# Kernel tuning notes

Measured on AMD Instinct MI355X. Metric: run time of the kernel, lower is better.

Reference implementation:

```python
import jax, jax.numpy as jnp
import numpy as np

DIM_V = 512
H = 8
EPS = 1e-5

def _layernorm(x, g, b):
    mu = jnp.mean(x, axis=-1, keepdims=True)
    var = jnp.var(x, axis=-1, keepdims=True)
    return (x - mu) * jax.lax.rsqrt(var + EPS) * g + b

def setup_inputs() -> dict:
    key = jax.random.key(0)
    ks = jax.random.split(key, 10)
    B, Nq, Nk, dq, dk, dv = 8, 1024, 1024, 512, 512, DIM_V
    def lin(k, fan_in, shape):
        bound = 1.0 / np.sqrt(fan_in)
        return jax.random.uniform(k, shape, jnp.float32, -bound, bound)
    return {
        "Q": jax.random.normal(ks[0], (B, Nq, dq), jnp.float32),
        "K": jax.random.normal(ks[1], (B, Nk, dk), jnp.float32),
        "Wq": lin(ks[2], dq, (dv, dq)), "bq": lin(ks[3], dq, (dv,)),
        "Wk": lin(ks[4], dk, (dv, dk)), "bk": lin(ks[5], dk, (dv,)),
        "Wv": lin(ks[6], dk, (dv, dk)), "bv": lin(ks[7], dk, (dv,)),
        "Wo": lin(ks[8], dv, (dv, dv)), "bo": lin(ks[9], dv, (dv,)),
        "g0": jnp.ones((dv,), jnp.float32), "beta0": jnp.zeros((dv,), jnp.float32),
        "g1": jnp.ones((dv,), jnp.float32), "beta1": jnp.zeros((dv,), jnp.float32),
    }

def reference(Q, K, Wq, bq, Wk, bk, Wv, bv, Wo, bo, g0, beta0, g1, beta1):
    B, Nq, _ = Q.shape
    Nk = K.shape[1]
    d_h = DIM_V // H
    Qp = Q @ Wq.T + bq            # [B,Nq,dv]
    Kp = K @ Wk.T + bk            # [B,Nk,dv]
    Vp = K @ Wv.T + bv            # [B,Nk,dv]
    # split heads along feature dim (matches torch split(dim_split,2)+cat(0))
    Qh = Qp.reshape(B, Nq, H, d_h).transpose(0, 2, 1, 3)  # [B,H,Nq,dh]
    Kh = Kp.reshape(B, Nk, H, d_h).transpose(0, 2, 1, 3)
    Vh = Vp.reshape(B, Nk, H, d_h).transpose(0, 2, 1, 3)
    # NOTE: original scales by sqrt(dim_V), the FULL model dim
    scores = jnp.einsum('bhnd,bhmd->bhnm', Qh, Kh) / jnp.sqrt(jnp.float32(DIM_V))
    A = jax.nn.softmax(scores, axis=-1)                   # [B,H,Nq,Nk]
    Oh = Qh + jnp.einsum('bhnm,bhmd->bhnd', A, Vh)        # residual on projected Q
    O = Oh.transpose(0, 2, 1, 3).reshape(B, Nq, DIM_V)
    O = _layernorm(O, g0, beta0)
    O = O + jax.nn.relu(O @ Wo.T + bo)
    O = _layernorm(O, g1, beta1)
    return O
```

## Files before the change

kernel.cpp:

```cpp
#include <hip/hip_runtime.h>
#include <hip/hip_bf16.h>

typedef __hip_bfloat16 bf16;
typedef short bf16x8 __attribute__((ext_vector_type(8)));
typedef float f32x4 __attribute__((ext_vector_type(4)));
typedef unsigned int u32;

static __device__ __forceinline__ float bfu2f(unsigned short u) { return __uint_as_float((u32)u << 16); }
static __device__ __forceinline__ u32 pack2(float a, float b) {
    return (u32)__bfloat16_as_ushort(__float2bfloat16(a))
         | ((u32)__bfloat16_as_ushort(__float2bfloat16(b)) << 16);
}
static __device__ __forceinline__ float wave_sum(float v) {
    #pragma unroll
    for (int off = 32; off > 0; off >>= 1) v += __shfl_xor(v, off);
    return v;
}

static __device__ __forceinline__ void gll16(const bf16* g, bf16* l) {
    __builtin_amdgcn_global_load_lds((const __attribute__((address_space(1))) void*)g,
                                     (__attribute__((address_space(3))) void*)l,
                                     16, 0, 0);
}

__global__ __launch_bounds__(256) void castall(const float* __restrict__ Q,  const float* __restrict__ K,
                                               const float* __restrict__ Wq, const float* __restrict__ Wk,
                                               const float* __restrict__ Wv, const float* __restrict__ Wo,
                                               bf16* __restrict__ dQ,  bf16* __restrict__ dK,
                                               bf16* __restrict__ dWq, bf16* __restrict__ dWk,
                                               bf16* __restrict__ dWv, bf16* __restrict__ dWo)
{
    const int b = blockIdx.x;
    const float* src; bf16* dst; size_t off;
    if (b < 1024)      { src = Q;  dst = dQ;  off = (size_t)b * 4096; }
    else if (b < 2048) { src = K;  dst = dK;  off = (size_t)(b - 1024) * 4096; }
    else {
        const int wb = b - 2048, wi = wb >> 6;
        off = (size_t)(wb & 63) * 4096;
        src = wi == 0 ? Wq : wi == 1 ? Wk : wi == 2 ? Wv : Wo;
        dst = wi == 0 ? dWq : wi == 1 ? dWk : wi == 2 ? dWv : dWo;
    }
    const size_t p = off + threadIdx.x * 16;
    const float4 v0 = *(const float4*)(src + p);
    const float4 v1 = *(const float4*)(src + p + 4);
    const float4 v2 = *(const float4*)(src + p + 8);
    const float4 v3 = *(const float4*)(src + p + 12);
    uint4 o0, o1;
    o0.x = pack2(v0.x, v0.y); o0.y = pack2(v0.z, v0.w);
    o0.z = pack2(v1.x, v1.y); o0.w = pack2(v1.z, v1.w);
    o1.x = pack2(v2.x, v2.y); o1.y = pack2(v2.z, v2.w);
    o1.z = pack2(v3.x, v3.y); o1.w = pack2(v3.z, v3.w);
    *(uint4*)(dst + p)     = o0;
    *(uint4*)(dst + p + 8) = o1;
}

__global__ __launch_bounds__(256) void gemm_qkv(const bf16* __restrict__ Aq, const bf16* __restrict__ Ak,
                                                const bf16* __restrict__ Wq, const bf16* __restrict__ Wk,
                                                const bf16* __restrict__ Wv,
                                                const float* __restrict__ bq, const float* __restrict__ bk,
                                                const float* __restrict__ bv,
                                                bf16* __restrict__ oQ, bf16* __restrict__ oK,
                                                bf16* __restrict__ oV)
{
    __shared__ bf16 Xs[128 * 64];
    __shared__ bf16 Ws[128 * 64];

    const int tid = threadIdx.x, lane = tid & 63, wave = tid >> 6;
    const int yy = blockIdx.y, wi = yy >> 2;
    const bf16* A     = wi == 0 ? Aq : Ak;
    const bf16* W     = wi == 0 ? Wq : wi == 1 ? Wk : Wv;
    const float* bias = wi == 0 ? bq : wi == 1 ? bk : bv;
    bf16* out         = wi == 0 ? oQ : wi == 1 ? oK : oV;
    const bool vmode  = (wi == 2);
    const int bm = blockIdx.x * 128;
    const int bn = (yy & 3) * 128;

    const int srow = tid >> 3;
    const int sg8  = (((tid & 7) ^ (srow & 7)) * 8);
    const int wm = (wave >> 1) * 64, wn = (wave & 1) * 64;
    const int fr = lane & 15, fq = lane >> 4;

    f32x4 acc[4][4] = {};
    const bf16* Ap = A + (size_t)(bm + srow) * 512 + sg8;
    const bf16* Wp = W + (size_t)(bn + srow) * 512 + sg8;
    const int ld = 8 * tid;

    for (int k0 = 0; k0 < 512; k0 += 64) {
        __syncthreads();
        #pragma unroll
        for (int c = 0; c < 4; c++) {
            gll16(Ap + k0 + (size_t)(32 * c) * 512, Xs + ld + 2048 * c);
            gll16(Wp + k0 + (size_t)(32 * c) * 512, Ws + ld + 2048 * c);
        }
        __syncthreads();

        #pragma unroll
        for (int c2 = 0; c2 < 2; c2++) {
            bf16x8 fx[4], fw[4];
            #pragma unroll
            for (int i = 0; i < 4; i++) {
                const int rx = wm + 16 * i + fr;
                const int rw = wn + 16 * i + fr;
                fx[i] = *(const bf16x8*)(&Xs[rx * 64 + (((c2 * 4 + fq) ^ (rx & 7)) * 8)]);
                fw[i] = *(const bf16x8*)(&Ws[rw * 64 + (((c2 * 4 + fq) ^ (rw & 7)) * 8)]);
            }
            if (vmode) {
                #pragma unroll
                for (int i = 0; i < 4; i++)
                    #pragma unroll
                    for (int j = 0; j < 4; j++)
                        acc[i][j] = __builtin_amdgcn_mfma_f32_16x16x32_bf16(fx[i], fw[j], acc[i][j], 0, 0, 0);
            } else {
                #pragma unroll
                for (int i = 0; i < 4; i++)
                    #pragma unroll
                    for (int j = 0; j < 4; j++)
                        acc[i][j] = __builtin_amdgcn_mfma_f32_16x16x32_bf16(fw[i], fx[j], acc[i][j], 0, 0, 0);
            }
        }
    }

    if (!vmode) {
        #pragma unroll
        for (int i = 0; i < 4; i++) {
            const int colb = bn + wn + 16 * i + 4 * fq;
            const float4 b4 = *(const float4*)(bias + colb);
            const int h = colb >> 6, d0 = colb & 63;
            #pragma unroll
            for (int j = 0; j < 4; j++) {
                const int n = bm + wm + 16 * j + fr;
                const int b = n >> 10, nn = n & 1023;
                uint2 pk;
                pk.x = pack2(acc[i][j][0] + b4.x, acc[i][j][1] + b4.y);
                pk.y = pack2(acc[i][j][2] + b4.z, acc[i][j][3] + b4.w);
                *(uint2*)(out + ((size_t)(b * 8 + h) * 1024 + nn) * 64 + d0) = pk;
            }
        }
    } else {
        #pragma unroll
        for (int i = 0; i < 4; i++) {
            const int n0 = bm + wm + 16 * i + 4 * fq;
            const int b = n0 >> 10, nn = n0 & 1023;
            #pragma unroll
            for (int j = 0; j < 4; j++) {
                const int col = bn + wn + 16 * j + fr;
                const float bv2 = bias[col];
                const int h = col >> 6, d = col & 63;
                uint2 pk;
                pk.x = pack2(acc[i][j][0] + bv2, acc[i][j][1] + bv2);
                pk.y = pack2(acc[i][j][2] + bv2, acc[i][j][3] + bv2);
                *(uint2*)(out + ((size_t)(b * 8 + h) * 64 + d) * 1024 + nn) = pk;
            }
        }
    }
}

__global__ __launch_bounds__(256) void gemm_o(const bf16* __restrict__ A,
                                              const bf16* __restrict__ W,
                                              const float* __restrict__ bias,
                                              bf16* __restrict__ out)
{
    __shared__ bf16 Xs[64 * 64];
    __shared__ bf16 Ws[128 * 64];

    const int tid = threadIdx.x, lane = tid & 63, wave = tid >> 6;
    const int bm = blockIdx.x * 64;
    const int bn = blockIdx.y * 128;

    const int srow = tid >> 3;
    const int sg8  = (((tid & 7) ^ (srow & 7)) * 8);
    const int wn = wave * 32;
    const int fr = lane & 15, fq = lane >> 4;

    f32x4 acc[2][4] = {};
    const bf16* Ap = A + (size_t)(bm + srow) * 512 + sg8;
    const bf16* Wp = W + (size_t)(bn + srow) * 512 + sg8;
    const int ld = 8 * tid;

    for (int k0 = 0; k0 < 512; k0 += 64) {
        __syncthreads();
        #pragma unroll
        for (int c = 0; c < 2; c++)
            gll16(Ap + k0 + (size_t)(32 * c) * 512, Xs + ld + 2048 * c);
        #pragma unroll
        for (int c = 0; c < 4; c++)
            gll16(Wp + k0 + (size_t)(32 * c) * 512, Ws + ld + 2048 * c);
        __syncthreads();

        #pragma unroll
        for (int c2 = 0; c2 < 2; c2++) {
            bf16x8 fx[4], fw[2];
            #pragma unroll
            for (int j = 0; j < 4; j++) {
                const int rx = 16 * j + fr;
                fx[j] = *(const bf16x8*)(&Xs[rx * 64 + (((c2 * 4 + fq) ^ (rx & 7)) * 8)]);
            }
            #pragma unroll
            for (int i = 0; i < 2; i++) {
                const int rw = wn + 16 * i + fr;
                fw[i] = *(const bf16x8*)(&Ws[rw * 64 + (((c2 * 4 + fq) ^ (rw & 7)) * 8)]);
            }
            #pragma unroll
            for (int i = 0; i < 2; i++)
                #pragma unroll
                for (int j = 0; j < 4; j++)
                    acc[i][j] = __builtin_amdgcn_mfma_f32_16x16x32_bf16(fw[i], fx[j], acc[i][j], 0, 0, 0);
        }
    }

    #pragma unroll
    for (int i = 0; i < 2; i++) {
        const int colb = bn + wn + 16 * i + 4 * fq;
        const float4 b4 = *(const float4*)(bias + colb);
        #pragma unroll
        for (int j = 0; j < 4; j++) {
            const int row = bm + 16 * j + fr;
            uint2 pk;
            pk.x = pack2(acc[i][j][0] + b4.x, acc[i][j][1] + b4.y);
            pk.y = pack2(acc[i][j][2] + b4.z, acc[i][j][3] + b4.w);
            *(uint2*)(out + (size_t)row * 512 + colb) = pk;
        }
    }
}

__global__ __launch_bounds__(256) void attn_mfma(const bf16* __restrict__ Qh,
                                                 const bf16* __restrict__ Kh,
                                                 const bf16* __restrict__ VhT,
                                                 bf16* __restrict__ Oc)
{
    __shared__ bf16 Ks[64 * 64];
    __shared__ bf16 Vs[64 * 64];
    __shared__ bf16 Ps[4][16 * 72];

    const int tid = threadIdx.x, lane = tid & 63, w = tid >> 6;
    const int id = blockIdx.x;
    const int bh = (id & 7) * 8 + (id >> 7);
    const int wq = ((id >> 3) & 15) * 64 + w * 16;

    const bf16* Qb = Qh  + ((size_t)bh * 1024 + wq) * 64;
    const bf16* Kb = Kh  + (size_t)bh * 1024 * 64;
    const bf16* Vb = VhT + (size_t)bh * 64 * 1024;

    const int fl = lane & 15, fq = lane >> 4;
    const int flk = fl & 7;
    const int gA = (fq ^ flk) * 8;
    const int gB = ((4 | fq) ^ flk) * 8;

    bf16x8 qf[2];
    qf[0] = *(const bf16x8*)(Qb + fl * 64 + fq * 8);
    qf[1] = *(const bf16x8*)(Qb + fl * 64 + 32 + fq * 8);

    f32x4 o[4] = {};
    float lsum = 0.f;
    const float sc2 = 0.04419417382415922f * 1.4426950408889634f;

    const int srow = tid >> 3;
    const int sg8  = (((tid & 7) ^ (srow & 7)) * 8);
    const bf16* KbR  = Kb + (size_t)srow * 64 + sg8;
    const bf16* VbR0 = Vb + (size_t)srow * 1024 + sg8;
    const bf16* VbR1 = Vb + (size_t)(srow + 32) * 1024 + sg8;
    const int ld = 8 * tid;

    for (int kt = 0; kt < 16; kt++) {
        const int m0 = kt * 64;
        __syncthreads();
        gll16(KbR + (size_t)m0 * 64,        Ks + ld);
        gll16(KbR + (size_t)(m0 + 32) * 64, Ks + 2048 + ld);
        gll16(VbR0 + m0,                    Vs + ld);
        gll16(VbR1 + m0,                    Vs + 2048 + ld);
        __syncthreads();

        bf16x8 kf[4][2];
        #pragma unroll
        for (int tm = 0; tm < 4; tm++) {
            kf[tm][0] = *(const bf16x8*)(&Ks[(16 * tm + fl) * 64 + gA]);
            kf[tm][1] = *(const bf16x8*)(&Ks[(16 * tm + fl) * 64 + gB]);
        }

        f32x4 st[4] = {};
        #pragma unroll
        for (int tm = 0; tm < 4; tm++) {
            st[tm] = __builtin_amdgcn_mfma_f32_16x16x32_bf16(kf[tm][0], qf[0], st[tm], 0, 0, 0);
            st[tm] = __builtin_amdgcn_mfma_f32_16x16x32_bf16(kf[tm][1], qf[1], st[tm], 0, 0, 0);
        }
        #pragma unroll
        for (int tm = 0; tm < 4; tm++) {
            float p0 = __builtin_amdgcn_exp2f(st[tm][0] * sc2);
            float p1 = __builtin_amdgcn_exp2f(st[tm][1] * sc2);
            float p2 = __builtin_amdgcn_exp2f(st[tm][2] * sc2);
            float p3 = __builtin_amdgcn_exp2f(st[tm][3] * sc2);
            lsum += (p0 + p1) + (p2 + p3);
            uint2 pk;
            pk.x = pack2(p0, p1);
            pk.y = pack2(p2, p3);
            *(uint2*)(&Ps[w][fl * 72 + 16 * tm + fq * 4]) = pk;
        }

        bf16x8 vf[4][2];
        #pragma unroll
        for (int jd = 0; jd < 4; jd++) {
            vf[jd][0] = *(const bf16x8*)(&Vs[(16 * jd + fl) * 64 + gA]);
            vf[jd][1] = *(const bf16x8*)(&Vs[(16 * jd + fl) * 64 + gB]);
        }
        bf16x8 pf0 = *(const bf16x8*)(&Ps[w][fl * 72 + fq * 8]);
        bf16x8 pf1 = *(const bf16x8*)(&Ps[w][fl * 72 + 32 + fq * 8]);
        #pragma unroll
        for (int jd = 0; jd < 4; jd++) {
            o[jd] = __builtin_amdgcn_mfma_f32_16x16x32_bf16(vf[jd][0], pf0, o[jd], 0, 0, 0);
            o[jd] = __builtin_amdgcn_mfma_f32_16x16x32_bf16(vf[jd][1], pf1, o[jd], 0, 0, 0);
        }
    }

    const int b = bh >> 3, h = bh & 7;
    float ls = lsum;
    ls += __shfl_xor(ls, 16);
    ls += __shfl_xor(ls, 32);
    const float linv = 1.f / ls;
    const size_t obase = ((size_t)(b * 1024 + wq + fl)) * 512 + h * 64;
    #pragma unroll
    for (int jd = 0; jd < 4; jd++) {
        const ushort4 qr = *(const ushort4*)(Qb + fl * 64 + 16 * jd + fq * 4);
        uint2 w2;
        w2.x = pack2(o[jd][0] * linv + bfu2f(qr.x), o[jd][1] * linv + bfu2f(qr.y));
        w2.y = pack2(o[jd][2] * linv + bfu2f(qr.z), o[jd][3] * linv + bfu2f(qr.w));
        *(uint2*)(&Oc[obase + 16 * jd + fq * 4]) = w2;
    }
}

__global__ __launch_bounds__(256) void ln0(const bf16* __restrict__ X,
                                           const float* __restrict__ g,
                                           const float* __restrict__ be,
                                           bf16* __restrict__ Y)
{
    const int lane = threadIdx.x & 63;
    const int row = blockIdx.x * 4 + (threadIdx.x >> 6);
    const size_t base = (size_t)row * 512 + lane * 8;
    const bf16x8 xv = *(const bf16x8*)(X + base);
    float x[8];
    #pragma unroll
    for (int j = 0; j < 8; j++) x[j] = bfu2f((unsigned short)xv[j]);
    float s = 0.f, s2 = 0.f;
    #pragma unroll
    for (int j = 0; j < 8; j++) { s += x[j]; s2 += x[j] * x[j]; }
    s = wave_sum(s); s2 = wave_sum(s2);
    const float mean = s * (1.f / 512.f);
    const float var = s2 * (1.f / 512.f) - mean * mean;
    const float rs = rsqrtf(fmaxf(var, 0.f) + 1e-5f);
    const float4 gv0 = *(const float4*)(g + lane * 8);
    const float4 gv1 = *(const float4*)(g + lane * 8 + 4);
    const float4 bv0 = *(const float4*)(be + lane * 8);
    const float4 bv1 = *(const float4*)(be + lane * 8 + 4);
    uint4 ov;
    ov.x = pack2((x[0]-mean)*rs*gv0.x + bv0.x, (x[1]-mean)*rs*gv0.y + bv0.y);
    ov.y = pack2((x[2]-mean)*rs*gv0.z + bv0.z, (x[3]-mean)*rs*gv0.w + bv0.w);
    ov.z = pack2((x[4]-mean)*rs*gv1.x + bv1.x, (x[5]-mean)*rs*gv1.y + bv1.y);
    ov.w = pack2((x[6]-mean)*rs*gv1.z + bv1.z, (x[7]-mean)*rs*gv1.w + bv1.w);
    *(uint4*)(Y + base) = ov;
}

__global__ __launch_bounds__(256) void ln1(const bf16* __restrict__ X,
                                           const bf16* __restrict__ R,
                                           const float* __restrict__ g,
                                           const float* __restrict__ be,
                                           float* __restrict__ Y)
{
    const int lane = threadIdx.x & 63;
    const int row = blockIdx.x * 4 + (threadIdx.x >> 6);
    const size_t base = (size_t)row * 512 + lane * 8;
    const bf16x8 xv = *(const bf16x8*)(X + base);
    const bf16x8 rv = *(const bf16x8*)(R + base);
    float x[8];
    #pragma unroll
    for (int j = 0; j < 8; j++)
        x[j] = bfu2f((unsigned short)rv[j]) + fmaxf(bfu2f((unsigned short)xv[j]), 0.f);
    float s = 0.f, s2 = 0.f;
    #pragma unroll
    for (int j = 0; j < 8; j++) { s += x[j]; s2 += x[j] * x[j]; }
    s = wave_sum(s); s2 = wave_sum(s2);
    const float mean = s * (1.f / 512.f);
    const float var = s2 * (1.f / 512.f) - mean * mean;
    const float rs = rsqrtf(fmaxf(var, 0.f) + 1e-5f);
    const float4 gv0 = *(const float4*)(g + lane * 8);
    const float4 gv1 = *(const float4*)(g + lane * 8 + 4);
    const float4 bv0 = *(const float4*)(be + lane * 8);
    const float4 bv1 = *(const float4*)(be + lane * 8 + 4);
    float4 y0, y1;
    y0.x = (x[0]-mean)*rs*gv0.x + bv0.x; y0.y = (x[1]-mean)*rs*gv0.y + bv0.y;
    y0.z = (x[2]-mean)*rs*gv0.z + bv0.z; y0.w = (x[3]-mean)*rs*gv0.w + bv0.w;
    y1.x = (x[4]-mean)*rs*gv1.x + bv1.x; y1.y = (x[5]-mean)*rs*gv1.y + bv1.y;
    y1.z = (x[6]-mean)*rs*gv1.z + bv1.z; y1.w = (x[7]-mean)*rs*gv1.w + bv1.w;
    *(float4*)(Y + base)     = y0;
    *(float4*)(Y + base + 4) = y1;
}

extern "C" void kernel_launch(void* const* d_in, const int* in_sizes, int n_in,
                              void* d_out, int out_size, void* d_ws, size_t ws_size,
                              hipStream_t stream)
{
    const float* Q   = (const float*)d_in[0];
    const float* K   = (const float*)d_in[1];
    const float* Wq  = (const float*)d_in[2];
    const float* bq  = (const float*)d_in[3];
    const float* Wk  = (const float*)d_in[4];
    const float* bk  = (const float*)d_in[5];
    const float* Wv  = (const float*)d_in[6];
    const float* bv  = (const float*)d_in[7];
    const float* Wo  = (const float*)d_in[8];
    const float* bo  = (const float*)d_in[9];
    const float* g0  = (const float*)d_in[10];
    const float* be0 = (const float*)d_in[11];
    const float* g1  = (const float*)d_in[12];
    const float* be1 = (const float*)d_in[13];
    float* out = (float*)d_out;

    const size_t NQK = (size_t)8 * 1024 * 512;
    const size_t NW  = (size_t)512 * 512;
    bf16* ws   = (bf16*)d_ws;
    bf16* cQ   = ws;
    bf16* cK   = cQ + NQK;
    bf16* cWq  = cK + NQK;
    bf16* cWk  = cWq + NW;
    bf16* cWv  = cWk + NW;
    bf16* cWo  = cWv + NW;
    bf16* pQh  = cWo + NW;
    bf16* pKh  = pQh + NQK;
    bf16* pVhT = pKh + NQK;
    bf16* pOc  = (bf16*)d_out;
    bf16* pO1  = pKh;
    bf16* pTmp = pQh;

    castall<<<2304, 256, 0, stream>>>(Q, K, Wq, Wk, Wv, Wo, cQ, cK, cWq, cWk, cWv, cWo);
    gemm_qkv<<<dim3(64, 12), 256, 0, stream>>>(cQ, cK, cWq, cWk, cWv, bq, bk, bv, pQh, pKh, pVhT);
    attn_mfma<<<1024, 256, 0, stream>>>(pQh, pKh, pVhT, pOc);
    ln0<<<2048, 256, 0, stream>>>(pOc, g0, be0, pO1);
    gemm_o<<<dim3(128, 4), 256, 0, stream>>>(pO1, cWo, bo, pTmp);
    ln1<<<2048, 256, 0, stream>>>(pTmp, pO1, g1, be1, out);
}
```

Measured before the change: 187.5 us.

## Fuse output projection GEMM with relu residual and final layernorm

```diff
diff --git a/kernel.cpp b/kernel.cpp
--- a/kernel.cpp
+++ b/kernel.cpp
@@ -151,74 +151,6 @@
                 pk.y = pack2(acc[i][j][2] + bv2, acc[i][j][3] + bv2);
                 *(uint2*)(out + ((size_t)(b * 8 + h) * 64 + d) * 1024 + nn) = pk;
             }
-        }
-    }
-}
-
-__global__ __launch_bounds__(256) void gemm_o(const bf16* __restrict__ A,
-                                              const bf16* __restrict__ W,
-                                              const float* __restrict__ bias,
-                                              bf16* __restrict__ out)
-{
-    __shared__ bf16 Xs[64 * 64];
-    __shared__ bf16 Ws[128 * 64];
-
-    const int tid = threadIdx.x, lane = tid & 63, wave = tid >> 6;
-    const int bm = blockIdx.x * 64;
-    const int bn = blockIdx.y * 128;
-
-    const int srow = tid >> 3;
-    const int sg8  = (((tid & 7) ^ (srow & 7)) * 8);
-    const int wn = wave * 32;
-    const int fr = lane & 15, fq = lane >> 4;
-
-    f32x4 acc[2][4] = {};
-    const bf16* Ap = A + (size_t)(bm + srow) * 512 + sg8;
-    const bf16* Wp = W + (size_t)(bn + srow) * 512 + sg8;
-    const int ld = 8 * tid;
-
-    for (int k0 = 0; k0 < 512; k0 += 64) {
-        __syncthreads();
-        #pragma unroll
-        for (int c = 0; c < 2; c++)
-            gll16(Ap + k0 + (size_t)(32 * c) * 512, Xs + ld + 2048 * c);
-        #pragma unroll
-        for (int c = 0; c < 4; c++)
-            gll16(Wp + k0 + (size_t)(32 * c) * 512, Ws + ld + 2048 * c);
-        __syncthreads();
-
-        #pragma unroll
-        for (int c2 = 0; c2 < 2; c2++) {
-            bf16x8 fx[4], fw[2];
-            #pragma unroll
-            for (int j = 0; j < 4; j++) {
-                const int rx = 16 * j + fr;
-                fx[j] = *(const bf16x8*)(&Xs[rx * 64 + (((c2 * 4 + fq) ^ (rx & 7)) * 8)]);
-            }
-            #pragma unroll
-            for (int i = 0; i < 2; i++) {
-                const int rw = wn + 16 * i + fr;
-                fw[i] = *(const bf16x8*)(&Ws[rw * 64 + (((c2 * 4 + fq) ^ (rw & 7)) * 8)]);
-            }
-            #pragma unroll
-            for (int i = 0; i < 2; i++)
-                #pragma unroll
-                for (int j = 0; j < 4; j++)
-                    acc[i][j] = __builtin_amdgcn_mfma_f32_16x16x32_bf16(fw[i], fx[j], acc[i][j], 0, 0, 0);
-        }
-    }
-
-    #pragma unroll
-    for (int i = 0; i < 2; i++) {
-        const int colb = bn + wn + 16 * i + 4 * fq;
-        const float4 b4 = *(const float4*)(bias + colb);
-        #pragma unroll
-        for (int j = 0; j < 4; j++) {
-            const int row = bm + 16 * j + fr;
-            uint2 pk;
-            pk.x = pack2(acc[i][j][0] + b4.x, acc[i][j][1] + b4.y);
-            pk.y = pack2(acc[i][j][2] + b4.z, acc[i][j][3] + b4.w);
-            *(uint2*)(out + (size_t)row * 512 + colb) = pk;
         }
     }
 }
@@ -358,39 +290,124 @@
     *(uint4*)(Y + base) = ov;
 }
 
-__global__ __launch_bounds__(256) void ln1(const bf16* __restrict__ X,
-                                           const bf16* __restrict__ R,
-                                           const float* __restrict__ g,
-                                           const float* __restrict__ be,
-                                           float* __restrict__ Y)
-{
-    const int lane = threadIdx.x & 63;
-    const int row = blockIdx.x * 4 + (threadIdx.x >> 6);
-    const size_t base = (size_t)row * 512 + lane * 8;
-    const bf16x8 xv = *(const bf16x8*)(X + base);
-    const bf16x8 rv = *(const bf16x8*)(R + base);
-    float x[8];
-    #pragma unroll
-    for (int j = 0; j < 8; j++)
-        x[j] = bfu2f((unsigned short)rv[j]) + fmaxf(bfu2f((unsigned short)xv[j]), 0.f);
-    float s = 0.f, s2 = 0.f;
-    #pragma unroll
-    for (int j = 0; j < 8; j++) { s += x[j]; s2 += x[j] * x[j]; }
-    s = wave_sum(s); s2 = wave_sum(s2);
-    const float mean = s * (1.f / 512.f);
-    const float var = s2 * (1.f / 512.f) - mean * mean;
-    const float rs = rsqrtf(fmaxf(var, 0.f) + 1e-5f);
-    const float4 gv0 = *(const float4*)(g + lane * 8);
-    const float4 gv1 = *(const float4*)(g + lane * 8 + 4);
-    const float4 bv0 = *(const float4*)(be + lane * 8);
-    const float4 bv1 = *(const float4*)(be + lane * 8 + 4);
-    float4 y0, y1;
-    y0.x = (x[0]-mean)*rs*gv0.x + bv0.x; y0.y = (x[1]-mean)*rs*gv0.y + bv0.y;
-    y0.z = (x[2]-mean)*rs*gv0.z + bv0.z; y0.w = (x[3]-mean)*rs*gv0.w + bv0.w;
-    y1.x = (x[4]-mean)*rs*gv1.x + bv1.x; y1.y = (x[5]-mean)*rs*gv1.y + bv1.y;
-    y1.z = (x[6]-mean)*rs*gv1.z + bv1.z; y1.w = (x[7]-mean)*rs*gv1.w + bv1.w;
-    *(float4*)(Y + base)     = y0;
-    *(float4*)(Y + base + 4) = y1;
+__global__ __launch_bounds__(512) void gemm_fo_ln1(const bf16* __restrict__ A,
+                                                   const bf16* __restrict__ W,
+                                                   const float* __restrict__ bo,
+                                                   const float* __restrict__ g1,
+                                                   const float* __restrict__ be1,
+                                                   float* __restrict__ out)
+{
+    __shared__ bf16 As[32 * 512];
+    __shared__ bf16 Ws[512 * 64];
+    __shared__ float2 red[32][8];
+
+    const int tid = threadIdx.x, lane = tid & 63, w = tid >> 6;
+    const int bm = blockIdx.x * 32;
+    const int wn = w * 64;
+    const int fr = lane & 15, fq = lane >> 4;
+
+    const int ldb = 8 * tid;
+    #pragma unroll
+    for (int c = 0; c < 4; c++) {
+        const int lin = tid + 512 * c;
+        const int row = lin >> 6, g = lin & 63;
+        gll16(A + (size_t)(bm + row) * 512 + ((g ^ (row & 7)) * 8),
+              As + ldb + 4096 * c);
+    }
+
+    const int srow = tid >> 3;
+    const int sg8  = (((tid & 7) ^ (srow & 7)) * 8);
+    const bf16* Wp = W + (size_t)srow * 512 + sg8;
+
+    f32x4 acc[4][2] = {};
+
+    for (int kt = 0; kt < 8; kt++) {
+        const int k0 = kt * 64;
+        if (kt) __syncthreads();
+        #pragma unroll
+        for (int c = 0; c < 8; c++)
+            gll16(Wp + k0 + (size_t)(64 * c) * 512, Ws + ldb + 4096 * c);
+        __syncthreads();
+
+        const int kb = kt * 8;
+        #pragma unroll
+        for (int c2 = 0; c2 < 2; c2++) {
+            bf16x8 fx[2], fw[4];
+            #pragma unroll
+            for (int j = 0; j < 2; j++) {
+                const int rx = 16 * j + fr;
+                fx[j] = *(const bf16x8*)(&As[rx * 512 + (kb + ((c2 * 4 + fq) ^ (rx & 7))) * 8]);
+            }
+            #pragma unroll
+            for (int i = 0; i < 4; i++) {
+                const int rw = wn + 16 * i + fr;
+                fw[i] = *(const bf16x8*)(&Ws[rw * 64 + (((c2 * 4 + fq) ^ (rw & 7)) * 8)]);
+            }
+            #pragma unroll
+            for (int i = 0; i < 4; i++)
+                #pragma unroll
+                for (int j = 0; j < 2; j++)
+                    acc[i][j] = __builtin_amdgcn_mfma_f32_16x16x32_bf16(fw[i], fx[j], acc[i][j], 0, 0, 0);
+        }
+    }
+
+    float yv[4][2][4];
+    float s[2] = {0.f, 0.f}, s2[2] = {0.f, 0.f};
+    #pragma unroll
+    for (int i = 0; i < 4; i++) {
+        const int c = wn + 16 * i + 4 * fq;
+        const float4 bo4 = *(const float4*)(bo + c);
+        const int gc = c >> 3, co = c & 7;
+        #pragma unroll
+        for (int j = 0; j < 2; j++) {
+            const int n = 16 * j + fr;
+            const ushort4 rr = *(const ushort4*)(&As[n * 512 + ((gc ^ (n & 7)) * 8 + co)]);
+            float y0 = bfu2f(rr.x) + fmaxf(acc[i][j][0] + bo4.x, 0.f);
+            float y1 = bfu2f(rr.y) + fmaxf(acc[i][j][1] + bo4.y, 0.f);
+            float y2 = bfu2f(rr.z) + fmaxf(acc[i][j][2] + bo4.z, 0.f);
+            float y3 = bfu2f(rr.w) + fmaxf(acc[i][j][3] + bo4.w, 0.f);
+            s[j]  += (y0 + y1) + (y2 + y3);
+            s2[j] += (y0 * y0 + y1 * y1) + (y2 * y2 + y3 * y3);
+            yv[i][j][0] = y0; yv[i][j][1] = y1; yv[i][j][2] = y2; yv[i][j][3] = y3;
+        }
+    }
+    #pragma unroll
+    for (int j = 0; j < 2; j++) {
+        s[j]  += __shfl_xor(s[j], 16);  s[j]  += __shfl_xor(s[j], 32);
+        s2[j] += __shfl_xor(s2[j], 16); s2[j] += __shfl_xor(s2[j], 32);
+    }
+    if (fq == 0) {
+        red[fr][w]      = make_float2(s[0], s2[0]);
+        red[16 + fr][w] = make_float2(s[1], s2[1]);
+    }
+    __syncthreads();
+    float mu[2], rs[2];
+    #pragma unroll
+    for (int j = 0; j < 2; j++) {
+        const int n = 16 * j + fr;
+        float S = 0.f, S2 = 0.f;
+        #pragma unroll
+        for (int q = 0; q < 8; q++) { const float2 v = red[n][q]; S += v.x; S2 += v.y; }
+        mu[j] = S * (1.f / 512.f);
+        const float var = S2 * (1.f / 512.f) - mu[j] * mu[j];
+        rs[j] = rsqrtf(fmaxf(var, 0.f) + 1e-5f);
+    }
+    #pragma unroll
+    for (int i = 0; i < 4; i++) {
+        const int c = wn + 16 * i + 4 * fq;
+        const float4 g4 = *(const float4*)(g1 + c);
+        const float4 b4 = *(const float4*)(be1 + c);
+        #pragma unroll
+        for (int j = 0; j < 2; j++) {
+            const int n = bm + 16 * j + fr;
+            float4 o4;
+            o4.x = (yv[i][j][0] - mu[j]) * rs[j] * g4.x + b4.x;
+            o4.y = (yv[i][j][1] - mu[j]) * rs[j] * g4.y + b4.y;
+            o4.z = (yv[i][j][2] - mu[j]) * rs[j] * g4.z + b4.z;
+            o4.w = (yv[i][j][3] - mu[j]) * rs[j] * g4.w + b4.w;
+            *(float4*)(out + (size_t)n * 512 + c) = o4;
+        }
+    }
 }
 
 extern "C" void kernel_launch(void* const* d_in, const int* in_sizes, int n_in,
@@ -427,12 +444,10 @@
     bf16* pVhT = pKh + NQK;
     bf16* pOc  = (bf16*)d_out;
     bf16* pO1  = pKh;
-    bf16* pTmp = pQh;
 
     castall<<<2304, 256, 0, stream>>>(Q, K, Wq, Wk, Wv, Wo, cQ, cK, cWq, cWk, cWv, cWo);
     gemm_qkv<<<dim3(64, 12), 256, 0, stream>>>(cQ, cK, cWq, cWk, cWv, bq, bk, bv, pQh, pKh, pVhT);
     attn_mfma<<<1024, 256, 0, stream>>>(pQh, pKh, pVhT, pOc);
     ln0<<<2048, 256, 0, stream>>>(pOc, g0, be0, pO1);
-    gemm_o<<<dim3(128, 4), 256, 0, stream>>>(pO1, cWo, bo, pTmp);
-    ln1<<<2048, 256, 0, stream>>>(pTmp, pO1, g1, be1, out);
-}
+    gemm_fo_ln1<<<256, 512, 0, stream>>>(pO1, cWo, bo, g1, be1, out);
+}
```

Result: no change. 186.3 us (-0.6%).
